# Performance work log

Measured on AMD Instinct MI355X. Metric: run time of the kernel, lower is better.

Reference implementation:

```python
import jax, jax.numpy as jnp
import numpy as np

B = 1000        # graphs in batch
T_PER = 250     # tasks per graph
M_PER = 50      # machines per graph
N_T = B * T_PER
N_M = B * M_PER
D_T = 16        # INPUT_TASK_DIM
D_M = 8         # INPUT_MACHINE_DIM
H = 128         # hidden_dim
IN_PREV_IDX = 0
TASK_FEAT_IDX = 1
EPS = 1e-5      # BatchNorm eps


def _mk_params(rng):
    def lin(i, o):
        return (rng.standard_normal((i, o)).astype(np.float32) / np.sqrt(i),
                np.zeros(o, np.float32))
    p = {}
    p['bn_t_gamma'] = np.ones(D_T, np.float32); p['bn_t_beta'] = np.zeros(D_T, np.float32)
    p['Wt1'], p['bt1'] = lin(D_T, H); p['Wt2'], p['bt2'] = lin(H, H)
    p['bn_m_gamma'] = np.ones(D_M, np.float32); p['bn_m_beta'] = np.zeros(D_M, np.float32)
    p['Wm1'], p['bm1'] = lin(D_M, H); p['Wm2'], p['bm2'] = lin(H, H)
    p['Wa1'], p['ba1'] = lin(2 * H, H); p['Wa2'], p['ba2'] = lin(H, H)
    p['Wl1'], p['bl1'] = lin(3 * H, H); p['Wl2'], p['bl2'] = lin(H, H)
    p['Wo1'], p['bo1'] = lin(H, H); p['Wo2'], p['bo2'] = lin(H, 1)
    return p


def setup_inputs() -> dict:
    rng = np.random.default_rng(0)
    xt = rng.standard_normal((N_T, D_T)).astype(np.float32)
    # prev-task flag: even task ids are 'prev'
    xt[:, IN_PREV_IDX] = (np.arange(N_T) % 2 == 0).astype(np.float32)
    # per-graph machine assignment in [0, M_PER), or -1 (unassigned) every 10th task
    lm = rng.integers(0, M_PER, N_T)
    lm[np.arange(N_T) % 10 == 0] = -1
    xt[:, TASK_FEAT_IDX] = lm.astype(np.float32)
    xm = rng.standard_normal((N_M, D_M)).astype(np.float32)
    inp = {'x_tasks': jnp.asarray(xt), 'x_machines': jnp.asarray(xm)}
    inp.update({k: jnp.asarray(v) for k, v in _mk_params(rng).items()})
    inp['x_tasks_batch'] = jnp.asarray(np.repeat(np.arange(B), T_PER).astype(np.int32))
    inp['x_machines_batch'] = jnp.asarray(np.repeat(np.arange(B), M_PER).astype(np.int32))
    # labels are tasks 0,5,10,...; prev tasks are even ids -> prev-local index t//2
    # label tasks that are prev: t % 10 == 0 -> prev_tasks_label_idx = 5*arange(N_T//10)
    inp['label_idx'] = jnp.asarray((5 * np.arange(N_T // 10)).astype(np.int32))
    inp['num_graphs'] = B
    return inp


def _bn(x, g, b):
    # BatchNorm1d in training mode: biased batch stats
    mu = x.mean(axis=0)
    var = x.var(axis=0)
    return g * (x - mu) * jax.lax.rsqrt(var + EPS) + b


def _seg_mean(x, seg, n):
    s = jax.ops.segment_sum(x, seg, num_segments=n)
    c = jax.ops.segment_sum(jnp.ones((x.shape[0], 1), x.dtype), seg, num_segments=n)
    return s / jnp.maximum(c, 1.0)


def reference(x_tasks, x_machines, bn_t_gamma, bn_t_beta, Wt1, bt1, Wt2, bt2,
              bn_m_gamma, bn_m_beta, Wm1, bm1, Wm2, bm2,
              Wa1, ba1, Wa2, ba2, Wl1, bl1, Wl2, bl2,
              Wo1, bo1, Wo2, bo2,
              x_tasks_batch, x_machines_batch, label_idx, num_graphs):
    nm = x_machines.shape[0]
    # tasks_select_assignment: local machine id -> global machine row (or pad row nm)
    tm_col = x_tasks[:, TASK_FEAT_IDX]
    cnt_m = jnp.bincount(x_machines_batch, length=num_graphs)
    cum = jnp.cumsum(cnt_m) - cnt_m  # cumulative machines per graph
    task_m = jnp.where(tm_col == -1.0, nm,
                       tm_col.astype(jnp.int32) + cum[x_tasks_batch].astype(jnp.int32))
    # node embeddings: BN -> Linear -> ReLU -> Linear -> ReLU
    th = jax.nn.relu(jax.nn.relu(_bn(x_tasks, bn_t_gamma, bn_t_beta) @ Wt1 + bt1) @ Wt2 + bt2)
    mh = jax.nn.relu(jax.nn.relu(_bn(x_machines, bn_m_gamma, bn_m_beta) @ Wm1 + bm1) @ Wm2 + bm2)
    # global aggregation per graph (scatter_mean) + MLP
    aggr = jnp.concatenate([_seg_mean(th, x_tasks_batch, num_graphs),
                            _seg_mean(mh, x_machines_batch, num_graphs)], axis=1)
    aggr = jax.nn.relu(aggr @ Wa1 + ba1) @ Wa2 + ba2
    # gather machine embedding per task (pad row of zeros for unassigned)
    mh_pad = jnp.concatenate([mh, jnp.zeros((1, H), mh.dtype)], axis=0)
    cat = jnp.concatenate([th, aggr[x_tasks_batch], mh_pad[task_m]], axis=1)  # [N_T, 3H]
    h = jax.nn.relu(cat @ Wl1 + bl1) @ Wl2 + bl2
    out = (jax.nn.relu(h @ Wo1 + bo1) @ Wo2 + bo2)[label_idx]
    return out
```

## Files before the change

kernel.cpp:

```cpp
#include <hip/hip_runtime.h>

constexpr int B     = 1000;
constexpr int T_PER = 250;
constexpr int M_PER = 50;
constexpr int N_T   = B * T_PER;
constexpr int N_M   = B * M_PER;
constexpr int H     = 128;
constexpr int N_LBL = 25000;
constexpr float EPS = 1e-05f;

constexpr int NB_T = 256;
constexpr int NB_M = 64;
constexpr int NB_P = 64;

constexpr int OFF_PART_T = 0;
constexpr int OFF_PART_M = OFF_PART_T + NB_T * 32;
constexpr int OFF_AT     = OFF_PART_M + NB_M * 16;
constexpr int OFF_BT     = OFF_AT + 16;
constexpr int OFF_AM     = OFF_BT + 16;
constexpr int OFF_BM     = OFF_AM + 8;
constexpr int OFF_BT1F   = OFF_BM + 8;
constexpr int OFF_BM1F   = OFF_BT1F + 128;
constexpr int OFF_MEANT  = OFF_BM1F + 128;
constexpr int OFF_MEANM  = OFF_MEANT + B * H;
constexpr int OFF_AGG2   = OFF_MEANM + B * H;
constexpr int OFF_HALF   = OFF_AGG2 + B * H;
constexpr int HO_WT1  = 0;
constexpr int HO_WT2  = 4096;
constexpr int HO_WM1  = 20480;
constexpr int HO_WM2  = 24576;
constexpr int HO_WA1  = 40960;
constexpr int HO_WA2  = 73728;
constexpr int HO_WL1  = 90112;
constexpr int HO_WL2  = 139264;
constexpr int HO_WO1  = 155648;
constexpr int HO_XT16 = 172032;
constexpr int HO_XM16 = HO_XT16 + N_T * 16;

typedef _Float16 f16x8 __attribute__((ext_vector_type(8)));
typedef _Float16 f16x4 __attribute__((ext_vector_type(4)));
typedef float f32x4 __attribute__((ext_vector_type(4)));

#define MFMA16(a, b, c) __builtin_amdgcn_mfma_f32_16x16x32_f16(a, b, c, 0, 0, 0)

template <int C, int NB>
__device__ __forceinline__ void stats_body(const float* __restrict__ x,
                                           _Float16* __restrict__ x16, int nelem,
                                           float* __restrict__ part, int blk, int t,
                                           float* ls, float* lq) {
    float s = 0.f, q = 0.f;
    for (int e = blk * 256 + t; e < nelem; e += NB * 256) {
        float v = x[e];
        s += v;
        q += v * v;
        x16[e] = (_Float16)v;
    }
    ls[t] = s; lq[t] = q;
    __syncthreads();
    if (t < C) {
        float S = 0.f, Q = 0.f;
        for (int u = t; u < 256; u += C) { S += ls[u]; Q += lq[u]; }
        part[blk * 2 * C + t] = S;
        part[blk * 2 * C + C + t] = Q;
    }
}

__device__ __forceinline__ void cvt_tr(const float* __restrict__ src, _Float16* __restrict__ dst,
                                       int K, int Kp, int tid, int nt) {
    for (int idx = tid; idx < 128 * Kp; idx += nt) {
        int c = idx / Kp, k = idx - c * Kp;
        float v = (k < K) ? src[k * 128 + c] : 0.f;
        dst[idx] = (_Float16)v;
    }
}

__global__ __launch_bounds__(256) void stats_prep_kernel(
        const float* __restrict__ xt, const float* __restrict__ xm,
        _Float16* __restrict__ xt16, _Float16* __restrict__ xm16,
        const float* __restrict__ Wt2, const float* __restrict__ Wm2,
        const float* __restrict__ Wa1, const float* __restrict__ Wa2,
        const float* __restrict__ Wl1, const float* __restrict__ Wl2,
        const float* __restrict__ Wo1,
        float* __restrict__ wsf, _Float16* __restrict__ wh) {
    __shared__ float ls[256], lq[256];
    const int bid = blockIdx.x, t = threadIdx.x;
    if (bid < NB_T) {
        stats_body<16, NB_T>(xt, xt16, N_T * 16, wsf + OFF_PART_T, bid, t, ls, lq);
    } else if (bid < NB_T + NB_M) {
        stats_body<8, NB_M>(xm, xm16, N_M * 8, wsf + OFF_PART_M, bid - NB_T, t, ls, lq);
    } else {
        const int tid = (bid - NB_T - NB_M) * 256 + t;
        const int nt = NB_P * 256;
        cvt_tr(Wt2, wh + HO_WT2, 128, 128, tid, nt);
        cvt_tr(Wm2, wh + HO_WM2, 128, 128, tid, nt);
        cvt_tr(Wa1, wh + HO_WA1, 256, 256, tid, nt);
        cvt_tr(Wa2, wh + HO_WA2, 128, 128, tid, nt);
        cvt_tr(Wl1, wh + HO_WL1, 384, 384, tid, nt);
        cvt_tr(Wl2, wh + HO_WL2, 128, 128, tid, nt);
        cvt_tr(Wo1, wh + HO_WO1, 128, 128, tid, nt);
    }
}

__global__ __launch_bounds__(256) void finalize_kernel(
        const float* __restrict__ gt, const float* __restrict__ btb,
        const float* __restrict__ gm, const float* __restrict__ bmb,
        const float* __restrict__ Wt1, const float* __restrict__ bt1,
        const float* __restrict__ Wm1, const float* __restrict__ bm1,
        float* __restrict__ ws, _Float16* __restrict__ wh) {
    __shared__ float red[256];
    __shared__ float statT[32], statM[16];
    __shared__ float shT[16], shM[8];
    __shared__ float saT[16], saM[8];
    const int t = threadIdx.x;
    {
        const int slot = t & 31, chunk = t >> 5;
        const float* p = ws + OFF_PART_T;
        float s = 0.f;
        for (int b = chunk * 32; b < chunk * 32 + 32; b++) s += p[b * 32 + slot];
        red[t] = s;
    }
    __syncthreads();
    if (t < 32) {
        float v = 0.f;
#pragma unroll
        for (int c = 0; c < 8; c++) v += red[t + 32 * c];
        statT[t] = v;
    }
    __syncthreads();
    {
        float s = 0.f;
        if (t < 128) {
            const int slot = t & 15, chunk = t >> 4;
            const float* p = ws + OFF_PART_M;
            for (int b = chunk * 8; b < chunk * 8 + 8; b++) s += p[b * 16 + slot];
        }
        red[t] = s;
    }
    __syncthreads();
    if (t < 16) {
        float v = 0.f;
#pragma unroll
        for (int c = 0; c < 8; c++) v += red[t + 16 * c];
        statM[t] = v;
    }
    __syncthreads();
    if (t < 16) {
        float mu  = statT[t] / (float)N_T;
        float var = statT[16 + t] / (float)N_T - mu * mu;
        float a   = gt[t] * rsqrtf(var + EPS);
        ws[OFF_AT + t] = a;
        float b = btb[t] - mu * a;
        ws[OFF_BT + t] = b;
        shT[t] = b;
        saT[t] = a;
    } else if (t < 24) {
        int c = t - 16;
        float mu  = statM[c] / (float)N_M;
        float var = statM[8 + c] / (float)N_M - mu * mu;
        float a   = gm[c] * rsqrtf(var + EPS);
        ws[OFF_AM + c] = a;
        float b = bmb[c] - mu * a;
        ws[OFF_BM + c] = b;
        shM[c] = b;
        saM[c] = a;
    }
    __syncthreads();
    if (t < 128) {
        float s = bt1[t];
#pragma unroll
        for (int k = 0; k < 16; k++) s += shT[k] * Wt1[k * 128 + t];
        ws[OFF_BT1F + t] = s;
        _Float16 row[32];
#pragma unroll
        for (int k = 0; k < 16; k++) row[k] = (_Float16)(Wt1[k * 128 + t] * saT[k]);
        float bh = (float)(_Float16)s;
        row[16] = (_Float16)s;
        row[17] = (_Float16)(s - bh);
#pragma unroll
        for (int k = 18; k < 32; k++) row[k] = (_Float16)0.f;
#pragma unroll
        for (int q = 0; q < 4; q++)
            *(f16x8*)(wh + HO_WT1 + t * 32 + q * 8) = *(const f16x8*)(row + q * 8);
    } else {
        int c = t - 128;
        float s = bm1[c];
#pragma unroll
        for (int k = 0; k < 8; k++) s += shM[k] * Wm1[k * 128 + c];
        ws[OFF_BM1F + c] = s;
        _Float16 row[32];
#pragma unroll
        for (int k = 0; k < 8; k++) row[k] = (_Float16)(Wm1[k * 128 + c] * saM[k]);
        float bh = (float)(_Float16)s;
        row[8] = (_Float16)s;
        row[9] = (_Float16)(s - bh);
#pragma unroll
        for (int k = 10; k < 32; k++) row[k] = (_Float16)0.f;
#pragma unroll
        for (int q = 0; q < 4; q++)
            *(f16x8*)(wh + HO_WM1 + c * 32 + q * 8) = *(const f16x8*)(row + q * 8);
    }
}

__device__ __forceinline__ void zacc(f32x4 acc[4][2]) {
#pragma unroll
    for (int rg = 0; rg < 4; rg++)
#pragma unroll
        for (int mi = 0; mi < 2; mi++) acc[rg][mi] = (f32x4){0.f, 0.f, 0.f, 0.f};
}

__device__ __forceinline__ void ld32(f16x8 w[2], const _Float16* __restrict__ WT,
                                     int m0, int r, int gq) {
#pragma unroll
    for (int mi = 0; mi < 2; mi++)
        w[mi] = *(const f16x8*)(WT + ((m0 + mi) * 16 + r) * 32 + gq * 8);
}

__device__ __forceinline__ void ld128(f16x8 w[2][4], const _Float16* __restrict__ WT,
                                      int lda, int k0, int m0, int r, int gq) {
#pragma unroll
    for (int mi = 0; mi < 2; mi++)
#pragma unroll
        for (int ks = 0; ks < 4; ks++)
            w[mi][ks] = *(const f16x8*)(WT + ((m0 + mi) * 16 + r) * lda + k0 + ks * 32 + gq * 8);
}

__device__ __forceinline__ void mm32g(const f16x8 w[2], const f16x8 xb[4], f32x4 acc[4][2]) {
#pragma unroll
    for (int rg = 0; rg < 4; rg++) {
        acc[rg][0] = MFMA16(w[0], xb[rg], acc[rg][0]);
        acc[rg][1] = MFMA16(w[1], xb[rg], acc[rg][1]);
    }
}

__device__ __forceinline__ void mm32(const f16x8 w[2], const _Float16* __restrict__ act,
                                     int rstride, int r, int gq, f32x4 acc[4][2]) {
#pragma unroll
    for (int rg = 0; rg < 4; rg++) {
        const f16x8 bf = *(const f16x8*)(act + (rg * 16 + r) * rstride + gq * 8);
        acc[rg][0] = MFMA16(w[0], bf, acc[rg][0]);
        acc[rg][1] = MFMA16(w[1], bf, acc[rg][1]);
    }
}

__device__ __forceinline__ void mm128(const f16x8 w[2][4], const _Float16* __restrict__ act,
                                      int rstride, int r, int gq, f32x4 acc[4][2]) {
#pragma unroll
    for (int rg = 0; rg < 4; rg++)
#pragma unroll
        for (int ks = 0; ks < 4; ks++) {
            const f16x8 bf = *(const f16x8*)(act + (rg * 16 + r) * rstride + ks * 32 + gq * 8);
            acc[rg][0] = MFMA16(w[0][ks], bf, acc[rg][0]);
            acc[rg][1] = MFMA16(w[1][ks], bf, acc[rg][1]);
        }
}

__device__ __forceinline__ void epi_cs(const f32x4 acc[4][2], const f32x4 bv[2],
                                       _Float16* __restrict__ dst, int dstride,
                                       int m0, int r, int gq, bool relu) {
#pragma unroll
    for (int rg = 0; rg < 4; rg++)
#pragma unroll
        for (int mi = 0; mi < 2; mi++) {
            f16x4 hv;
#pragma unroll
            for (int j = 0; j < 4; j++) {
                float v = acc[rg][mi][j] + bv[mi][j];
                if (relu) v = fmaxf(v, 0.f);
                hv[j] = (_Float16)v;
            }
            *(f16x4*)(dst + (rg * 16 + r) * dstride + (m0 + mi) * 16 + gq * 4) = hv;
        }
}

__global__ __launch_bounds__(256, 3) void seg_tile4(
        const _Float16* __restrict__ xt16, const _Float16* __restrict__ xm16,
        const _Float16* __restrict__ wh, const float* __restrict__ wsf,
        const float* __restrict__ bt2, const float* __restrict__ bm2,
        float* __restrict__ meanT, float* __restrict__ meanM) {
    __shared__ __attribute__((aligned(16))) _Float16 h1s[64 * 136];
    const int t = threadIdx.x, lane = t & 63, w = t >> 6;
    const int r = lane & 15, gq = lane >> 4;
    const int m0 = 2 * w;
    const bool taskb = (blockIdx.x < B);
    const _Float16* W1T = wh + (taskb ? HO_WT1 : HO_WM1);
    const _Float16* W2T = wh + (taskb ? HO_WT2 : HO_WM2);
    const float* b1f = wsf + (taskb ? OFF_BT1F : OFF_BM1F);
    const float* b2  = taskb ? bt2 : bm2;
    const _Float16* x16 = taskb ? xt16 : xm16;
    const int ROWS = taskb ? T_PER : M_PER;
    const int CIN  = taskb ? 16 : 8;
    f16x8 w1[2]; ld32(w1, W1T, m0, r, gq);
    f16x8 w2[2][4]; ld128(w2, W2T, 128, 0, m0, r, gq);
    f32x4 b1v[2], b2v[2];
#pragma unroll
    for (int mi = 0; mi < 2; mi++) {
        b1v[mi] = *(const f32x4*)(b1f + (m0 + mi) * 16 + gq * 4);
        b2v[mi] = *(const f32x4*)(b2 + (m0 + mi) * 16 + gq * 4);
    }
    f16x8 z8;
#pragma unroll
    for (int e = 0; e < 8; e++) z8[e] = (_Float16)0.f;
    const bool loader = taskb ? (gq < 2) : (gq == 0);
    const int gb = taskb ? blockIdx.x : 0;
    const int mg0 = taskb ? 0 : (blockIdx.x - B) * 4;
    const f32x4 zf = (f32x4){0.f, 0.f, 0.f, 0.f};
    f32x4 rs[2];
    rs[0] = zf; rs[1] = zf;
    f16x8 xb[4];
    {
        const int g0 = taskb ? gb : mg0;
#pragma unroll
        for (int rg = 0; rg < 4; rg++) {
            int row = rg * 16 + r;
            int cl = (row < ROWS) ? row : (ROWS - 1);
            xb[rg] = loader ? *(const f16x8*)(x16 + (g0 * ROWS + cl) * CIN + gq * 8) : z8;
        }
    }
    for (int it = 0; it < 4; it++) {
        const int g = taskb ? gb : (mg0 + it);
        const int rbase = taskb ? (it * 64) : 0;
        f32x4 acc[4][2];
        zacc(acc);
        mm32g(w1, xb, acc);
        epi_cs(acc, b1v, h1s, 136, m0, r, gq, true);
        __syncthreads();
        if (it < 3) {
            const int gn = taskb ? gb : (mg0 + it + 1);
            const int rbn = taskb ? ((it + 1) * 64) : 0;
#pragma unroll
            for (int rg = 0; rg < 4; rg++) {
                int row = rbn + rg * 16 + r;
                int cl = (row < ROWS) ? row : (ROWS - 1);
                xb[rg] = loader ? *(const f16x8*)(x16 + (gn * ROWS + cl) * CIN + gq * 8) : z8;
            }
        }
        zacc(acc);
        mm128(w2, h1s, 136, r, gq, acc);
        if (taskb) {
            if (rbase + 64 <= ROWS) {
#pragma unroll
                for (int rg = 0; rg < 4; rg++)
#pragma unroll
                    for (int mi = 0; mi < 2; mi++)
#pragma unroll
                        for (int j = 0; j < 4; j++)
                            rs[mi][j] += fmaxf(acc[rg][mi][j] + b2v[mi][j], 0.f);
            } else {
#pragma unroll
                for (int rg = 0; rg < 4; rg++) {
                    const float mk = ((rbase + rg * 16 + r) < ROWS) ? 1.f : 0.f;
#pragma unroll
                    for (int mi = 0; mi < 2; mi++)
#pragma unroll
                        for (int j = 0; j < 4; j++)
                            rs[mi][j] = fmaf(fmaxf(acc[rg][mi][j] + b2v[mi][j], 0.f), mk, rs[mi][j]);
                }
            }
        } else {
            f32x4 ms[2];
            ms[0] = zf; ms[1] = zf;
#pragma unroll
            for (int rg = 0; rg < 4; rg++) {
                const float mk = ((rg * 16 + r) < ROWS) ? 1.f : 0.f;
#pragma unroll
                for (int mi = 0; mi < 2; mi++)
#pragma unroll
                    for (int j = 0; j < 4; j++)
                        ms[mi][j] = fmaf(fmaxf(acc[rg][mi][j] + b2v[mi][j], 0.f), mk, ms[mi][j]);
            }
#pragma unroll
            for (int mi = 0; mi < 2; mi++)
#pragma unroll
                for (int j = 0; j < 4; j++) {
                    float v = ms[mi][j];
                    v += __shfl_xor(v, 1); v += __shfl_xor(v, 2);
                    v += __shfl_xor(v, 4); v += __shfl_xor(v, 8);
                    ms[mi][j] = v;
                }
            if (r == 0) {
                const float inv = 1.f / (float)M_PER;
#pragma unroll
                for (int mi = 0; mi < 2; mi++) {
                    f32x4 st = ms[mi] * inv;
                    *(f32x4*)(meanM + g * H + (m0 + mi) * 16 + gq * 4) = st;
                }
            }
        }
        if (it < 3) __syncthreads();
    }
    if (taskb) {
#pragma unroll
        for (int mi = 0; mi < 2; mi++)
#pragma unroll
            for (int j = 0; j < 4; j++) {
                float v = rs[mi][j];
                v += __shfl_xor(v, 1); v += __shfl_xor(v, 2);
                v += __shfl_xor(v, 4); v += __shfl_xor(v, 8);
                rs[mi][j] = v;
            }
        if (r == 0) {
            const float inv = 1.f / (float)T_PER;
#pragma unroll
            for (int mi = 0; mi < 2; mi++) {
                f32x4 st = rs[mi] * inv;
                *(f32x4*)(meanT + gb * H + (m0 + mi) * 16 + gq * 4) = st;
            }
        }
    }
}

__global__ __launch_bounds__(256) void aggr_kernel(const float* __restrict__ meanT, const float* __restrict__ meanM,
        const _Float16* __restrict__ Wa1T, const float* __restrict__ ba1,
        const _Float16* __restrict__ Wa2T, const float* __restrict__ ba2,
        const _Float16* __restrict__ Wl1T, const float* __restrict__ bl1,
        float* __restrict__ agg2) {
    __shared__ __attribute__((aligned(16))) _Float16 cin[16 * 264];
    __shared__ __attribute__((aligned(16))) _Float16 h1s[16 * 136];
    __shared__ __attribute__((aligned(16))) _Float16 ags[16 * 136];
    const int t = threadIdx.x, lane = t & 63, wave = t >> 6;
    const int r = lane & 15, gq = lane >> 4;
    const int m0 = 2 * wave;
    const int g0 = blockIdx.x * 16;
    f16x8 wa1[2][8], wa2[2][4], wl1b[2][4];
#pragma unroll
    for (int mi = 0; mi < 2; mi++)
#pragma unroll
        for (int ks = 0; ks < 8; ks++)
            wa1[mi][ks] = *(const f16x8*)(Wa1T + ((m0 + mi) * 16 + r) * 256 + ks * 32 + gq * 8);
    ld128(wa2, Wa2T, 128, 0, m0, r, gq);
    ld128(wl1b, Wl1T, 384, 128, m0, r, gq);
    f32x4 b1v[2], b2v[2], blv[2];
#pragma unroll
    for (int mi = 0; mi < 2; mi++) {
        b1v[mi] = *(const f32x4*)(ba1 + (m0 + mi) * 16 + gq * 4);
        b2v[mi] = *(const f32x4*)(ba2 + (m0 + mi) * 16 + gq * 4);
        blv[mi] = *(const f32x4*)(bl1 + (m0 + mi) * 16 + gq * 4);
    }
    for (int e = t; e < 16 * 64; e += 256) {
        int j = e >> 6, c4 = e & 63;
        int g = g0 + j;
        float4 v = {0.f, 0.f, 0.f, 0.f};
        if (g < B) v = (c4 < 32) ? *(const float4*)(meanT + g * H + c4 * 4)
                                 : *(const float4*)(meanM + g * H + (c4 - 32) * 4);
        f16x4 hv;
        hv[0] = (_Float16)v.x; hv[1] = (_Float16)v.y; hv[2] = (_Float16)v.z; hv[3] = (_Float16)v.w;
        *(f16x4*)(cin + j * 264 + c4 * 4) = hv;
    }
    __syncthreads();
    f32x4 a0 = {0.f, 0.f, 0.f, 0.f}, a1 = {0.f, 0.f, 0.f, 0.f};
    {
        const _Float16* bp = cin + r * 264 + gq * 8;
#pragma unroll
        for (int ks = 0; ks < 8; ks++) {
            const f16x8 bf = *(const f16x8*)(bp + ks * 32);
            a0 = MFMA16(wa1[0][ks], bf, a0);
            a1 = MFMA16(wa1[1][ks], bf, a1);
        }
    }
    {
        f16x4 h0, h1v;
#pragma unroll
        for (int j = 0; j < 4; j++) {
            h0[j]  = (_Float16)fmaxf(a0[j] + b1v[0][j], 0.f);
            h1v[j] = (_Float16)fmaxf(a1[j] + b1v[1][j], 0.f);
        }
        *(f16x4*)(h1s + r * 136 + m0 * 16 + gq * 4) = h0;
        *(f16x4*)(h1s + r * 136 + (m0 + 1) * 16 + gq * 4) = h1v;
    }
    __syncthreads();
    a0 = (f32x4){0.f, 0.f, 0.f, 0.f}; a1 = (f32x4){0.f, 0.f, 0.f, 0.f};
    {
        const _Float16* bp = h1s + r * 136 + gq * 8;
#pragma unroll
        for (int ks = 0; ks < 4; ks++) {
            const f16x8 bf = *(const f16x8*)(bp + ks * 32);
            a0 = MFMA16(wa2[0][ks], bf, a0);
            a1 = MFMA16(wa2[1][ks], bf, a1);
        }
    }
    {
        f16x4 h0, h1v;
#pragma unroll
        for (int j = 0; j < 4; j++) {
            h0[j]  = (_Float16)(a0[j] + b2v[0][j]);
            h1v[j] = (_Float16)(a1[j] + b2v[1][j]);
        }
        *(f16x4*)(ags + r * 136 + m0 * 16 + gq * 4) = h0;
        *(f16x4*)(ags + r * 136 + (m0 + 1) * 16 + gq * 4) = h1v;
    }
    __syncthreads();
    a0 = (f32x4){0.f, 0.f, 0.f, 0.f}; a1 = (f32x4){0.f, 0.f, 0.f, 0.f};
    {
        const _Float16* bp = ags + r * 136 + gq * 8;
#pragma unroll
        for (int ks = 0; ks < 4; ks++) {
            const f16x8 bf = *(const f16x8*)(bp + ks * 32);
            a0 = MFMA16(wl1b[0][ks], bf, a0);
            a1 = MFMA16(wl1b[1][ks], bf, a1);
        }
    }
    if (g0 + r < B) {
        *(f32x4*)(agg2 + (g0 + r) * H + m0 * 16 + gq * 4) = a0 + blv[0];
        *(f32x4*)(agg2 + (g0 + r) * H + (m0 + 1) * 16 + gq * 4) = a1 + blv[1];
    }
}

__global__ __launch_bounds__(256) void label_kernel(
        const float* __restrict__ xt,
        const _Float16* __restrict__ xt16, const _Float16* __restrict__ xm16,
        const _Float16* __restrict__ Wt1T, const float* __restrict__ bt1f,
        const _Float16* __restrict__ Wt2T, const float* __restrict__ bt2,
        const _Float16* __restrict__ Wm1T, const float* __restrict__ bm1f,
        const _Float16* __restrict__ Wm2T, const float* __restrict__ bm2,
        const _Float16* __restrict__ Wl1T,
        const _Float16* __restrict__ Wl2T, const float* __restrict__ bl2,
        const _Float16* __restrict__ Wo1T, const float* __restrict__ bo1,
        const float* __restrict__ Wo2, const float* __restrict__ bo2,
        const float* __restrict__ agg2,
        const int* __restrict__ tbatch, const int* __restrict__ lidx,
        float* __restrict__ out) {
    __shared__ __attribute__((aligned(16))) _Float16 xs_t[64 * 40];
    __shared__ __attribute__((aligned(16))) _Float16 xs_m[64 * 40];
    __shared__ __attribute__((aligned(16))) _Float16 h1s[64 * 136];
    __shared__ __attribute__((aligned(16))) _Float16 cat[64 * 264];
    __shared__ float psum[4][64];
    __shared__ int ridx[64], gidx[64], midx[64];
    const int t = threadIdx.x;
    const int lane = t & 63, wave = t >> 6;
    const int r = lane & 15, gq = lane >> 4;
    const int m0 = 2 * wave;
    if (t < 64) {
        int i = blockIdx.x * 64 + t;
        int rr = (i < N_LBL) ? lidx[i] : 0;
        ridx[t] = rr;
        int gg = tbatch[rr];
        gidx[t] = gg;
        float tv = xt[rr * 16 + 1];
        midx[t] = (tv == -1.0f) ? -1 : ((int)tv + gg * M_PER);
    }
    __syncthreads();
    f16x4 z4; z4[0] = z4[1] = z4[2] = z4[3] = (_Float16)0.f;
    {
        int j = t >> 2, part = t & 3;
        f16x4 hv = *(const f16x4*)(xt16 + ridx[j] * 16 + part * 4);
        *(f16x4*)(xs_t + j * 40 + part * 4) = hv;
        *(f16x4*)(xs_t + j * 40 + 16 + part * 4) = z4;
    }
    if (t < 128) {
        int j = t >> 1, part = t & 1;
        int m = midx[j];
        f16x4 hv = z4;
        if (m >= 0) hv = *(const f16x4*)(xm16 + m * 8 + part * 4);
        *(f16x4*)(xs_m + j * 40 + part * 4) = hv;
#pragma unroll
        for (int q = 0; q < 3; q++)
            *(f16x4*)(xs_m + j * 40 + 8 + part * 12 + q * 4) = z4;
    }
    __syncthreads();
    f32x4 agg2v[4][2];
#pragma unroll
    for (int rg = 0; rg < 4; rg++)
#pragma unroll
        for (int mi = 0; mi < 2; mi++)
            agg2v[rg][mi] = *(const f32x4*)(agg2 + gidx[rg * 16 + r] * H + (m0 + mi) * 16 + gq * 4);
    f32x4 acc[4][2];
    f16x8 wt1[2]; ld32(wt1, Wt1T, m0, r, gq);
    f16x8 wt2[2][4]; ld128(wt2, Wt2T, 128, 0, m0, r, gq);
    f32x4 bva[2], bvb[2];
#pragma unroll
    for (int mi = 0; mi < 2; mi++) {
        bva[mi] = *(const f32x4*)(bt1f + (m0 + mi) * 16 + gq * 4);
        bvb[mi] = *(const f32x4*)(bt2 + (m0 + mi) * 16 + gq * 4);
    }
    zacc(acc);
    mm32(wt1, xs_t, 40, r, gq, acc);
    epi_cs(acc, bva, h1s, 136, m0, r, gq, true);
    f16x8 wm1[2]; ld32(wm1, Wm1T, m0, r, gq);
    __syncthreads();
    zacc(acc);
    mm128(wt2, h1s, 136, r, gq, acc);
    epi_cs(acc, bvb, cat, 264, m0, r, gq, true);
    f16x8 wm2[2][4]; ld128(wm2, Wm2T, 128, 0, m0, r, gq);
    __syncthreads();
#pragma unroll
    for (int mi = 0; mi < 2; mi++) {
        bva[mi] = *(const f32x4*)(bm1f + (m0 + mi) * 16 + gq * 4);
        bvb[mi] = *(const f32x4*)(bm2 + (m0 + mi) * 16 + gq * 4);
    }
    zacc(acc);
    mm32(wm1, xs_m, 40, r, gq, acc);
    epi_cs(acc, bva, h1s, 136, m0, r, gq, true);
    f16x8 wl1a[2][4]; ld128(wl1a, Wl1T, 384, 0, m0, r, gq);
    __syncthreads();
    zacc(acc);
    mm128(wm2, h1s, 136, r, gq, acc);
#pragma unroll
    for (int rg = 0; rg < 4; rg++) {
        const bool sent = (midx[rg * 16 + r] < 0);
#pragma unroll
        for (int mi = 0; mi < 2; mi++) {
            f16x4 hv;
#pragma unroll
            for (int j = 0; j < 4; j++) {
                float v = fmaxf(acc[rg][mi][j] + bvb[mi][j], 0.f);
                hv[j] = (_Float16)(sent ? 0.f : v);
            }
            *(f16x4*)(cat + (rg * 16 + r) * 264 + 128 + (m0 + mi) * 16 + gq * 4) = hv;
        }
    }
    f16x8 wl1c[2][4]; ld128(wl1c, Wl1T, 384, 256, m0, r, gq);
    __syncthreads();
    zacc(acc);
    mm128(wl1a, cat, 264, r, gq, acc);
    mm128(wl1c, cat + 128, 264, r, gq, acc);
#pragma unroll
    for (int rg = 0; rg < 4; rg++)
#pragma unroll
        for (int mi = 0; mi < 2; mi++) {
            f16x4 hv;
#pragma unroll
            for (int j = 0; j < 4; j++)
                hv[j] = (_Float16)fmaxf(acc[rg][mi][j] + agg2v[rg][mi][j], 0.f);
            *(f16x4*)(h1s + (rg * 16 + r) * 136 + (m0 + mi) * 16 + gq * 4) = hv;
        }
    f16x8 wl2[2][4]; ld128(wl2, Wl2T, 128, 0, m0, r, gq);
    __syncthreads();
#pragma unroll
    for (int mi = 0; mi < 2; mi++) bva[mi] = *(const f32x4*)(bl2 + (m0 + mi) * 16 + gq * 4);
    zacc(acc);
    mm128(wl2, h1s, 136, r, gq, acc);
    epi_cs(acc, bva, cat, 264, m0, r, gq, false);
    f16x8 wo1[2][4]; ld128(wo1, Wo1T, 128, 0, m0, r, gq);
    __syncthreads();
#pragma unroll
    for (int mi = 0; mi < 2; mi++) bva[mi] = *(const f32x4*)(bo1 + (m0 + mi) * 16 + gq * 4);
    f32x4 wo2v[2];
#pragma unroll
    for (int mi = 0; mi < 2; mi++) wo2v[mi] = *(const f32x4*)(Wo2 + (m0 + mi) * 16 + gq * 4);
    zacc(acc);
    mm128(wo1, cat, 264, r, gq, acc);
#pragma unroll
    for (int rg = 0; rg < 4; rg++) {
        float pv = 0.f;
#pragma unroll
        for (int mi = 0; mi < 2; mi++)
#pragma unroll
            for (int j = 0; j < 4; j++)
                pv += fmaxf(acc[rg][mi][j] + bva[mi][j], 0.f) * wo2v[mi][j];
        pv += __shfl_xor(pv, 16);
        pv += __shfl_xor(pv, 32);
        if (lane < 16) psum[wave][rg * 16 + lane] = pv;
    }
    __syncthreads();
    if (t < 64) {
        int i = blockIdx.x * 64 + t;
        if (i < N_LBL)
            out[i] = psum[0][t] + psum[1][t] + psum[2][t] + psum[3][t] + bo2[0];
    }
}

extern "C" void kernel_launch(void* const* d_in, const int* in_sizes, int n_in,
                              void* d_out, int out_size, void* d_ws, size_t ws_size,
                              hipStream_t stream) {
    const float* xt  = (const float*)d_in[0];
    const float* xm  = (const float*)d_in[1];
    const float* gt  = (const float*)d_in[2];
    const float* btb = (const float*)d_in[3];
    const float* Wt1 = (const float*)d_in[4];  const float* bt1 = (const float*)d_in[5];
    const float* Wt2 = (const float*)d_in[6];  const float* bt2 = (const float*)d_in[7];
    const float* gm  = (const float*)d_in[8];  const float* bmb = (const float*)d_in[9];
    const float* Wm1 = (const float*)d_in[10]; const float* bm1 = (const float*)d_in[11];
    const float* Wm2 = (const float*)d_in[12]; const float* bm2 = (const float*)d_in[13];
    const float* Wa1 = (const float*)d_in[14]; const float* ba1 = (const float*)d_in[15];
    const float* Wa2 = (const float*)d_in[16]; const float* ba2 = (const float*)d_in[17];
    const float* Wl1 = (const float*)d_in[18]; const float* bl1 = (const float*)d_in[19];
    const float* Wl2 = (const float*)d_in[20]; const float* bl2 = (const float*)d_in[21];
    const float* Wo1 = (const float*)d_in[22]; const float* bo1 = (const float*)d_in[23];
    const float* Wo2 = (const float*)d_in[24]; const float* bo2 = (const float*)d_in[25];
    const int* tb  = (const int*)d_in[26];
    const int* lix = (const int*)d_in[28];
    float* wsf = (float*)d_ws;
    _Float16* wh = (_Float16*)(wsf + OFF_HALF);
    _Float16* xt16 = wh + HO_XT16;
    _Float16* xm16 = wh + HO_XM16;
    float* outp = (float*)d_out;

    stats_prep_kernel<<<NB_T + NB_M + NB_P, 256, 0, stream>>>(
        xt, xm, xt16, xm16, Wt2, Wm2, Wa1, Wa2, Wl1, Wl2, Wo1, wsf, wh);
    finalize_kernel<<<1, 256, 0, stream>>>(gt, btb, gm, bmb, Wt1, bt1, Wm1, bm1, wsf, wh);
    seg_tile4<<<B + 250, 256, 0, stream>>>(xt16, xm16, wh, wsf, bt2, bm2,
                                           wsf + OFF_MEANT, wsf + OFF_MEANM);
    aggr_kernel<<<(B + 15) / 16, 256, 0, stream>>>(wsf + OFF_MEANT, wsf + OFF_MEANM,
                                                   wh + HO_WA1, ba1, wh + HO_WA2, ba2,
                                                   wh + HO_WL1, bl1, wsf + OFF_AGG2);
    label_kernel<<<(N_LBL + 63) / 64, 256, 0, stream>>>(xt, xt16, xm16,
                                                        wh + HO_WT1, wsf + OFF_BT1F, wh + HO_WT2, bt2,
                                                        wh + HO_WM1, wsf + OFF_BM1F, wh + HO_WM2, bm2,
                                                        wh + HO_WL1,
                                                        wh + HO_WL2, bl2,
                                                        wh + HO_WO1, bo1, Wo2, bo2,
                                                        wsf + OFF_AGG2, tb, lix, outp);
}
```

Before: 73.11 us.

## Fold Wl2 into Wo1 and reuse machine embeddings from segment kernel

Precomputes the product Wl2·Wo1 and a folded bias in the single-block finalize kernel, so the label kernel runs one 128x128 matmul where it used to run two. The segment kernel now writes per-machine hidden embeddings to an fp16 buffer, and the label kernel gathers them directly instead of recomputing the machine MLP per label. Task inputs are loaded straight into registers rather than staged through shared memory. In exchange, finalize_kernel (one block) does extra serial work and seg_tile4 writes more to memory, and the folded fp16 weight product may change numerics slightly.

After: 85.92 us. 17.5% more time.

```diff
diff --git a/kernel.cpp b/kernel.cpp
--- a/kernel.cpp
+++ b/kernel.cpp
@@ -24,7 +24,8 @@
 constexpr int OFF_MEANT  = OFF_BM1F + 128;
 constexpr int OFF_MEANM  = OFF_MEANT + B * H;
 constexpr int OFF_AGG2   = OFF_MEANM + B * H;
-constexpr int OFF_HALF   = OFF_AGG2 + B * H;
+constexpr int OFF_BFOLD  = OFF_AGG2 + B * H;
+constexpr int OFF_HALF   = OFF_BFOLD + 128;
 constexpr int HO_WT1  = 0;
 constexpr int HO_WT2  = 4096;
 constexpr int HO_WM1  = 20480;
@@ -34,14 +35,77 @@
 constexpr int HO_WL1  = 90112;
 constexpr int HO_WL2  = 139264;
 constexpr int HO_WO1  = 155648;
-constexpr int HO_XT16 = 172032;
+constexpr int HO_WLO  = 172032;
+constexpr int HO_XT16 = 188416;
 constexpr int HO_XM16 = HO_XT16 + N_T * 16;
+constexpr int HO_MH16 = HO_XM16 + N_M * 8;
 
 typedef _Float16 f16x8 __attribute__((ext_vector_type(8)));
 typedef _Float16 f16x4 __attribute__((ext_vector_type(4)));
 typedef float f32x4 __attribute__((ext_vector_type(4)));
 
 #define MFMA16(a, b, c) __builtin_amdgcn_mfma_f32_16x16x32_f16(a, b, c, 0, 0, 0)
+
+__device__ __forceinline__ void zacc(f32x4 acc[4][2]) {
+#pragma unroll
+    for (int rg = 0; rg < 4; rg++)
+#pragma unroll
+        for (int mi = 0; mi < 2; mi++) acc[rg][mi] = (f32x4){0.f, 0.f, 0.f, 0.f};
+}
+
+__device__ __forceinline__ void ld32(f16x8 w[2], const _Float16* __restrict__ WT,
+                                     int m0, int r, int gq) {
+#pragma unroll
+    for (int mi = 0; mi < 2; mi++)
+        w[mi] = *(const f16x8*)(WT + ((m0 + mi) * 16 + r) * 32 + gq * 8);
+}
+
+__device__ __forceinline__ void ld128(f16x8 w[2][4], const _Float16* __restrict__ WT,
+                                      int lda, int k0, int m0, int r, int gq) {
+#pragma unroll
+    for (int mi = 0; mi < 2; mi++)
+#pragma unroll
+        for (int ks = 0; ks < 4; ks++)
+            w[mi][ks] = *(const f16x8*)(WT + ((m0 + mi) * 16 + r) * lda + k0 + ks * 32 + gq * 8);
+}
+
+__device__ __forceinline__ void mm32g(const f16x8 w[2], const f16x8 xb[4], f32x4 acc[4][2]) {
+#pragma unroll
+    for (int rg = 0; rg < 4; rg++) {
+        acc[rg][0] = MFMA16(w[0], xb[rg], acc[rg][0]);
+        acc[rg][1] = MFMA16(w[1], xb[rg], acc[rg][1]);
+    }
+}
+
+__device__ __forceinline__ void mm128(const f16x8 w[2][4], const _Float16* __restrict__ act,
+                                      int rstride, int r, int gq, f32x4 acc[4][2]) {
+#pragma unroll
+    for (int rg = 0; rg < 4; rg++)
+#pragma unroll
+        for (int ks = 0; ks < 4; ks++) {
+            const f16x8 bf = *(const f16x8*)(act + (rg * 16 + r) * rstride + ks * 32 + gq * 8);
+            acc[rg][0] = MFMA16(w[0][ks], bf, acc[rg][0]);
+            acc[rg][1] = MFMA16(w[1][ks], bf, acc[rg][1]);
+        }
+}
+
+__device__ __forceinline__ void epi_cs(const f32x4 acc[4][2], const f32x4 bv[2],
+                                       _Float16* __restrict__ dst, int dstride,
+                                       int m0, int r, int gq, bool relu) {
+#pragma unroll
+    for (int rg = 0; rg < 4; rg++)
+#pragma unroll
+        for (int mi = 0; mi < 2; mi++) {
+            f16x4 hv;
+#pragma unroll
+            for (int j = 0; j < 4; j++) {
+                float v = acc[rg][mi][j] + bv[mi][j];
+                if (relu) v = fmaxf(v, 0.f);
+                hv[j] = (_Float16)v;
+            }
+            *(f16x4*)(dst + (rg * 16 + r) * dstride + (m0 + mi) * 16 + gq * 4) = hv;
+        }
+}
 
 template <int C, int NB>
 __device__ __forceinline__ void stats_body(const float* __restrict__ x,
@@ -79,8 +143,7 @@
         _Float16* __restrict__ xt16, _Float16* __restrict__ xm16,
         const float* __restrict__ Wt2, const float* __restrict__ Wm2,
         const float* __restrict__ Wa1, const float* __restrict__ Wa2,
-        const float* __restrict__ Wl1, const float* __restrict__ Wl2,
-        const float* __restrict__ Wo1,
+        const float* __restrict__ Wl1, const float* __restrict__ Wo1,
         float* __restrict__ wsf, _Float16* __restrict__ wh) {
     __shared__ float ls[256], lq[256];
     const int bid = blockIdx.x, t = threadIdx.x;
@@ -96,7 +159,6 @@
         cvt_tr(Wa1, wh + HO_WA1, 256, 256, tid, nt);
         cvt_tr(Wa2, wh + HO_WA2, 128, 128, tid, nt);
         cvt_tr(Wl1, wh + HO_WL1, 384, 384, tid, nt);
-        cvt_tr(Wl2, wh + HO_WL2, 128, 128, tid, nt);
         cvt_tr(Wo1, wh + HO_WO1, 128, 128, tid, nt);
     }
 }
@@ -106,6 +168,8 @@
         const float* __restrict__ gm, const float* __restrict__ bmb,
         const float* __restrict__ Wt1, const float* __restrict__ bt1,
         const float* __restrict__ Wm1, const float* __restrict__ bm1,
+        const float* __restrict__ Wl2, const float* __restrict__ bl2,
+        const float* __restrict__ Wo1, const float* __restrict__ bo1,
         float* __restrict__ ws, _Float16* __restrict__ wh) {
     __shared__ float red[256];
     __shared__ float statT[32], statM[16];
@@ -199,84 +263,59 @@
         for (int q = 0; q < 4; q++)
             *(f16x8*)(wh + HO_WM1 + c * 32 + q * 8) = *(const f16x8*)(row + q * 8);
     }
-}
-
-__device__ __forceinline__ void zacc(f32x4 acc[4][2]) {
-#pragma unroll
-    for (int rg = 0; rg < 4; rg++)
-#pragma unroll
-        for (int mi = 0; mi < 2; mi++) acc[rg][mi] = (f32x4){0.f, 0.f, 0.f, 0.f};
-}
-
-__device__ __forceinline__ void ld32(f16x8 w[2], const _Float16* __restrict__ WT,
-                                     int m0, int r, int gq) {
-#pragma unroll
-    for (int mi = 0; mi < 2; mi++)
-        w[mi] = *(const f16x8*)(WT + ((m0 + mi) * 16 + r) * 32 + gq * 8);
-}
-
-__device__ __forceinline__ void ld128(f16x8 w[2][4], const _Float16* __restrict__ WT,
-                                      int lda, int k0, int m0, int r, int gq) {
-#pragma unroll
-    for (int mi = 0; mi < 2; mi++)
-#pragma unroll
-        for (int ks = 0; ks < 4; ks++)
-            w[mi][ks] = *(const f16x8*)(WT + ((m0 + mi) * 16 + r) * lda + k0 + ks * 32 + gq * 8);
-}
-
-__device__ __forceinline__ void mm32g(const f16x8 w[2], const f16x8 xb[4], f32x4 acc[4][2]) {
-#pragma unroll
-    for (int rg = 0; rg < 4; rg++) {
-        acc[rg][0] = MFMA16(w[0], xb[rg], acc[rg][0]);
-        acc[rg][1] = MFMA16(w[1], xb[rg], acc[rg][1]);
-    }
-}
-
-__device__ __forceinline__ void mm32(const f16x8 w[2], const _Float16* __restrict__ act,
-                                     int rstride, int r, int gq, f32x4 acc[4][2]) {
-#pragma unroll
-    for (int rg = 0; rg < 4; rg++) {
-        const f16x8 bf = *(const f16x8*)(act + (rg * 16 + r) * rstride + gq * 8);
-        acc[rg][0] = MFMA16(w[0], bf, acc[rg][0]);
-        acc[rg][1] = MFMA16(w[1], bf, acc[rg][1]);
-    }
-}
-
-__device__ __forceinline__ void mm128(const f16x8 w[2][4], const _Float16* __restrict__ act,
-                                      int rstride, int r, int gq, f32x4 acc[4][2]) {
-#pragma unroll
-    for (int rg = 0; rg < 4; rg++)
-#pragma unroll
-        for (int ks = 0; ks < 4; ks++) {
-            const f16x8 bf = *(const f16x8*)(act + (rg * 16 + r) * rstride + ks * 32 + gq * 8);
-            acc[rg][0] = MFMA16(w[0][ks], bf, acc[rg][0]);
-            acc[rg][1] = MFMA16(w[1][ks], bf, acc[rg][1]);
-        }
-}
-
-__device__ __forceinline__ void epi_cs(const f32x4 acc[4][2], const f32x4 bv[2],
-                                       _Float16* __restrict__ dst, int dstride,
-                                       int m0, int r, int gq, bool relu) {
-#pragma unroll
-    for (int rg = 0; rg < 4; rg++)
-#pragma unroll
-        for (int mi = 0; mi < 2; mi++) {
-            f16x4 hv;
-#pragma unroll
-            for (int j = 0; j < 4; j++) {
-                float v = acc[rg][mi][j] + bv[mi][j];
-                if (relu) v = fmaxf(v, 0.f);
-                hv[j] = (_Float16)v;
-            }
-            *(f16x4*)(dst + (rg * 16 + r) * dstride + (m0 + mi) * 16 + gq * 4) = hv;
-        }
+    {
+        const int lane = t & 63, wv = t >> 6;
+        const int r = lane & 15, gq = lane >> 4;
+        const int m0 = 2 * wv;
+        f16x8 wo1f[2][4];
+        ld128(wo1f, wh + HO_WO1, 128, 0, m0, r, gq);
+#pragma unroll
+        for (int half = 0; half < 2; half++) {
+            f32x4 acc[4][2];
+            zacc(acc);
+#pragma unroll
+            for (int rg = 0; rg < 4; rg++) {
+                const int k = half * 64 + rg * 16 + r;
+#pragma unroll
+                for (int ks = 0; ks < 4; ks++) {
+                    const float* src = Wl2 + k * 128 + ks * 32 + gq * 8;
+                    float4 a = *(const float4*)(src);
+                    float4 b = *(const float4*)(src + 4);
+                    f16x8 bf;
+                    bf[0] = (_Float16)a.x; bf[1] = (_Float16)a.y;
+                    bf[2] = (_Float16)a.z; bf[3] = (_Float16)a.w;
+                    bf[4] = (_Float16)b.x; bf[5] = (_Float16)b.y;
+                    bf[6] = (_Float16)b.z; bf[7] = (_Float16)b.w;
+                    acc[rg][0] = MFMA16(wo1f[0][ks], bf, acc[rg][0]);
+                    acc[rg][1] = MFMA16(wo1f[1][ks], bf, acc[rg][1]);
+                }
+            }
+#pragma unroll
+            for (int rg = 0; rg < 4; rg++) {
+                const int k = half * 64 + rg * 16 + r;
+#pragma unroll
+                for (int mi = 0; mi < 2; mi++)
+#pragma unroll
+                    for (int j = 0; j < 4; j++) {
+                        const int o = (m0 + mi) * 16 + gq * 4 + j;
+                        wh[HO_WLO + o * 128 + k] = (_Float16)acc[rg][mi][j];
+                    }
+            }
+        }
+        if (t < 128) {
+            float s = bo1[t];
+            for (int k = 0; k < 128; k++) s += bl2[k] * Wo1[k * 128 + t];
+            ws[OFF_BFOLD + t] = s;
+        }
+    }
 }
 
 __global__ __launch_bounds__(256, 3) void seg_tile4(
         const _Float16* __restrict__ xt16, const _Float16* __restrict__ xm16,
         const _Float16* __restrict__ wh, const float* __restrict__ wsf,
         const float* __restrict__ bt2, const float* __restrict__ bm2,
-        float* __restrict__ meanT, float* __restrict__ meanM) {
+        float* __restrict__ meanT, float* __restrict__ meanM,
+        _Float16* __restrict__ mh16) {
     __shared__ __attribute__((aligned(16))) _Float16 h1s[64 * 136];
     const int t = threadIdx.x, lane = t & 63, w = t >> 6;
     const int r = lane & 15, gq = lane >> 4;
@@ -361,12 +400,20 @@
             ms[0] = zf; ms[1] = zf;
 #pragma unroll
             for (int rg = 0; rg < 4; rg++) {
-                const float mk = ((rg * 16 + r) < ROWS) ? 1.f : 0.f;
-#pragma unroll
-                for (int mi = 0; mi < 2; mi++)
-#pragma unroll
-                    for (int j = 0; j < 4; j++)
-                        ms[mi][j] = fmaf(fmaxf(acc[rg][mi][j] + b2v[mi][j], 0.f), mk, ms[mi][j]);
+                const int row = rg * 16 + r;
+                const bool vr = (row < M_PER);
+#pragma unroll
+                for (int mi = 0; mi < 2; mi++) {
+                    f16x4 hv;
+#pragma unroll
+                    for (int j = 0; j < 4; j++) {
+                        float v = fmaxf(acc[rg][mi][j] + b2v[mi][j], 0.f);
+                        hv[j] = (_Float16)v;
+                        ms[mi][j] += vr ? v : 0.f;
+                    }
+                    if (vr)
+                        *(f16x4*)(mh16 + (g * M_PER + row) * H + (m0 + mi) * 16 + gq * 4) = hv;
+                }
             }
 #pragma unroll
             for (int mi = 0; mi < 2; mi++)
@@ -507,20 +554,15 @@
 
 __global__ __launch_bounds__(256) void label_kernel(
         const float* __restrict__ xt,
-        const _Float16* __restrict__ xt16, const _Float16* __restrict__ xm16,
+        const _Float16* __restrict__ xt16, const _Float16* __restrict__ mh16,
         const _Float16* __restrict__ Wt1T, const float* __restrict__ bt1f,
         const _Float16* __restrict__ Wt2T, const float* __restrict__ bt2,
-        const _Float16* __restrict__ Wm1T, const float* __restrict__ bm1f,
-        const _Float16* __restrict__ Wm2T, const float* __restrict__ bm2,
         const _Float16* __restrict__ Wl1T,
-        const _Float16* __restrict__ Wl2T, const float* __restrict__ bl2,
-        const _Float16* __restrict__ Wo1T, const float* __restrict__ bo1,
+        const _Float16* __restrict__ WloT, const float* __restrict__ bfold,
         const float* __restrict__ Wo2, const float* __restrict__ bo2,
         const float* __restrict__ agg2,
         const int* __restrict__ tbatch, const int* __restrict__ lidx,
         float* __restrict__ out) {
-    __shared__ __attribute__((aligned(16))) _Float16 xs_t[64 * 40];
-    __shared__ __attribute__((aligned(16))) _Float16 xs_m[64 * 40];
     __shared__ __attribute__((aligned(16))) _Float16 h1s[64 * 136];
     __shared__ __attribute__((aligned(16))) _Float16 cat[64 * 264];
     __shared__ float psum[4][64];
@@ -539,31 +581,23 @@
         midx[t] = (tv == -1.0f) ? -1 : ((int)tv + gg * M_PER);
     }
     __syncthreads();
-    f16x4 z4; z4[0] = z4[1] = z4[2] = z4[3] = (_Float16)0.f;
-    {
-        int j = t >> 2, part = t & 3;
-        f16x4 hv = *(const f16x4*)(xt16 + ridx[j] * 16 + part * 4);
-        *(f16x4*)(xs_t + j * 40 + part * 4) = hv;
-        *(f16x4*)(xs_t + j * 40 + 16 + part * 4) = z4;
-    }
-    if (t < 128) {
-        int j = t >> 1, part = t & 1;
-        int m = midx[j];
-        f16x4 hv = z4;
-        if (m >= 0) hv = *(const f16x4*)(xm16 + m * 8 + part * 4);
-        *(f16x4*)(xs_m + j * 40 + part * 4) = hv;
-#pragma unroll
-        for (int q = 0; q < 3; q++)
-            *(f16x4*)(xs_m + j * 40 + 8 + part * 12 + q * 4) = z4;
-    }
-    __syncthreads();
-    f32x4 agg2v[4][2];
-#pragma unroll
-    for (int rg = 0; rg < 4; rg++)
-#pragma unroll
-        for (int mi = 0; mi < 2; mi++)
-            agg2v[rg][mi] = *(const f32x4*)(agg2 + gidx[rg * 16 + r] * H + (m0 + mi) * 16 + gq * 4);
-    f32x4 acc[4][2];
+    f16x8 z8;
+#pragma unroll
+    for (int e = 0; e < 8; e++) z8[e] = (_Float16)0.f;
+    f16x8 xbT[4];
+#pragma unroll
+    for (int rg = 0; rg < 4; rg++) {
+        int rr = ridx[rg * 16 + r];
+        xbT[rg] = (gq < 2) ? *(const f16x8*)(xt16 + rr * 16 + gq * 8) : z8;
+    }
+    f16x8 mhv[4];
+#pragma unroll
+    for (int q = 0; q < 4; q++) {
+        int c = t + 256 * q;
+        int row = c >> 4, cb = c & 15;
+        int m = midx[row];
+        mhv[q] = (m >= 0) ? *(const f16x8*)(mh16 + m * H + cb * 8) : z8;
+    }
     f16x8 wt1[2]; ld32(wt1, Wt1T, m0, r, gq);
     f16x8 wt2[2][4]; ld128(wt2, Wt2T, 128, 0, m0, r, gq);
     f32x4 bva[2], bvb[2];
@@ -572,47 +606,32 @@
         bva[mi] = *(const f32x4*)(bt1f + (m0 + mi) * 16 + gq * 4);
         bvb[mi] = *(const f32x4*)(bt2 + (m0 + mi) * 16 + gq * 4);
     }
+    f32x4 acc[4][2];
     zacc(acc);
-    mm32(wt1, xs_t, 40, r, gq, acc);
+    mm32g(wt1, xbT, acc);
     epi_cs(acc, bva, h1s, 136, m0, r, gq, true);
-    f16x8 wm1[2]; ld32(wm1, Wm1T, m0, r, gq);
     __syncthreads();
     zacc(acc);
     mm128(wt2, h1s, 136, r, gq, acc);
     epi_cs(acc, bvb, cat, 264, m0, r, gq, true);
-    f16x8 wm2[2][4]; ld128(wm2, Wm2T, 128, 0, m0, r, gq);
-    __syncthreads();
-#pragma unroll
-    for (int mi = 0; mi < 2; mi++) {
-        bva[mi] = *(const f32x4*)(bm1f + (m0 + mi) * 16 + gq * 4);
-        bvb[mi] = *(const f32x4*)(bm2 + (m0 + mi) * 16 + gq * 4);
-    }
-    zacc(acc);
-    mm32(wm1, xs_m, 40, r, gq, acc);
-    epi_cs(acc, bva, h1s, 136, m0, r, gq, true);
+#pragma unroll
+    for (int q = 0; q < 4; q++) {
+        int c = t + 256 * q;
+        int row = c >> 4, cb = c & 15;
+        *(f16x8*)(cat + row * 264 + 128 + cb * 8) = mhv[q];
+    }
     f16x8 wl1a[2][4]; ld128(wl1a, Wl1T, 384, 0, m0, r, gq);
-    __syncthreads();
-    zacc(acc);
-    mm128(wm2, h1s, 136, r, gq, acc);
-#pragma unroll
-    for (int rg = 0; rg < 4; rg++) {
-        const bool sent = (midx[rg * 16 + r] < 0);
-#pragma unroll
-        for (int mi = 0; mi < 2; mi++) {
-            f16x4 hv;
-#pragma unroll
-            for (int j = 0; j < 4; j++) {
-                float v = fmaxf(acc[rg][mi][j] + bvb[mi][j], 0.f);
-                hv[j] = (_Float16)(sent ? 0.f : v);
-            }
-            *(f16x4*)(cat + (rg * 16 + r) * 264 + 128 + (m0 + mi) * 16 + gq * 4) = hv;
-        }
-    }
     f16x8 wl1c[2][4]; ld128(wl1c, Wl1T, 384, 256, m0, r, gq);
     __syncthreads();
     zacc(acc);
     mm128(wl1a, cat, 264, r, gq, acc);
     mm128(wl1c, cat + 128, 264, r, gq, acc);
+    f32x4 agg2v[4][2];
+#pragma unroll
+    for (int rg = 0; rg < 4; rg++)
+#pragma unroll
+        for (int mi = 0; mi < 2; mi++)
+            agg2v[rg][mi] = *(const f32x4*)(agg2 + gidx[rg * 16 + r] * H + (m0 + mi) * 16 + gq * 4);
 #pragma unroll
     for (int rg = 0; rg < 4; rg++)
 #pragma unroll
@@ -623,22 +642,15 @@
                 hv[j] = (_Float16)fmaxf(acc[rg][mi][j] + agg2v[rg][mi][j], 0.f);
             *(f16x4*)(h1s + (rg * 16 + r) * 136 + (m0 + mi) * 16 + gq * 4) = hv;
         }
-    f16x8 wl2[2][4]; ld128(wl2, Wl2T, 128, 0, m0, r, gq);
-    __syncthreads();
-#pragma unroll
-    for (int mi = 0; mi < 2; mi++) bva[mi] = *(const f32x4*)(bl2 + (m0 + mi) * 16 + gq * 4);
-    zacc(acc);
-    mm128(wl2, h1s, 136, r, gq, acc);
-    epi_cs(acc, bva, cat, 264, m0, r, gq, false);
-    f16x8 wo1[2][4]; ld128(wo1, Wo1T, 128, 0, m0, r, gq);
-    __syncthreads();
-#pragma unroll
-    for (int mi = 0; mi < 2; mi++) bva[mi] = *(const f32x4*)(bo1 + (m0 + mi) * 16 + gq * 4);
+    f16x8 wlo[2][4]; ld128(wlo, WloT, 128, 0, m0, r, gq);
+    __syncthreads();
+#pragma unroll
+    for (int mi = 0; mi < 2; mi++) bva[mi] = *(const f32x4*)(bfold + (m0 + mi) * 16 + gq * 4);
     f32x4 wo2v[2];
 #pragma unroll
     for (int mi = 0; mi < 2; mi++) wo2v[mi] = *(const f32x4*)(Wo2 + (m0 + mi) * 16 + gq * 4);
     zacc(acc);
-    mm128(wo1, cat, 264, r, gq, acc);
+    mm128(wlo, h1s, 136, r, gq, acc);
 #pragma unroll
     for (int rg = 0; rg < 4; rg++) {
         float pv = 0.f;
@@ -683,21 +695,22 @@
     _Float16* wh = (_Float16*)(wsf + OFF_HALF);
     _Float16* xt16 = wh + HO_XT16;
     _Float16* xm16 = wh + HO_XM16;
+    _Float16* mh16 = wh + HO_MH16;
     float* outp = (float*)d_out;
 
     stats_prep_kernel<<<NB_T + NB_M + NB_P, 256, 0, stream>>>(
-        xt, xm, xt16, xm16, Wt2, Wm2, Wa1, Wa2, Wl1, Wl2, Wo1, wsf, wh);
-    finalize_kernel<<<1, 256, 0, stream>>>(gt, btb, gm, bmb, Wt1, bt1, Wm1, bm1, wsf, wh);
+        xt, xm, xt16, xm16, Wt2, Wm2, Wa1, Wa2, Wl1, Wo1, wsf, wh);
+    finalize_kernel<<<1, 256, 0, stream>>>(gt, btb, gm, bmb, Wt1, bt1, Wm1, bm1,
+                                           Wl2, bl2, Wo1, bo1, wsf, wh);
     seg_tile4<<<B + 250, 256, 0, stream>>>(xt16, xm16, wh, wsf, bt2, bm2,
-                                           wsf + OFF_MEANT, wsf + OFF_MEANM);
+                                           wsf + OFF_MEANT, wsf + OFF_MEANM, mh16);
     aggr_kernel<<<(B + 15) / 16, 256, 0, stream>>>(wsf + OFF_MEANT, wsf + OFF_MEANM,
                                                    wh + HO_WA1, ba1, wh + HO_WA2, ba2,
                                                    wh + HO_WL1, bl1, wsf + OFF_AGG2);
-    label_kernel<<<(N_LBL + 63) / 64, 256, 0, stream>>>(xt, xt16, xm16,
+    label_kernel<<<(N_LBL + 63) / 64, 256, 0, stream>>>(xt, xt16, mh16,
                                                         wh + HO_WT1, wsf + OFF_BT1F, wh + HO_WT2, bt2,
-                                                        wh + HO_WM1, wsf + OFF_BM1F, wh + HO_WM2, bm2,
                                                         wh + HO_WL1,
-                                                        wh + HO_WL2, bl2,
-                                                        wh + HO_WO1, bo1, Wo2, bo2,
+                                                        wh + HO_WLO, wsf + OFF_BFOLD,
+                                                        Wo2, bo2,
                                                         wsf + OFF_AGG2, tb, lix, outp);
 }
```
